# Kernel optimization log

Measured on AMD Instinct MI355X. Metric: run time of the kernel, lower is better.

Reference implementation:

```python
import jax, jax.numpy as jnp
import numpy as np

B, S, H = 2, 1024, 2048
NH, NKV, HD = 16, 4, 128           # heads, kv heads, head_dim
E, TOPK, NG, TOPKG, M = 8, 2, 4, 2, 512  # experts, top_k, n_group, topk_group, moe ffn dim
EPS = 1e-6
THETA = 10000.0
SCALE = HD ** -0.5
RSF = 1.0  # routed_scaling_factor


def rmsnorm(x, w):
    xf = x.astype(jnp.float32)
    var = jnp.mean(xf * xf, axis=-1, keepdims=True)
    return (w * (xf * jax.lax.rsqrt(var + EPS))).astype(x.dtype)


def rotate_half(x):
    x1, x2 = jnp.split(x, 2, axis=-1)
    return jnp.concatenate([-x2, x1], axis=-1)


def setup_inputs() -> dict:
    key = jax.random.key(0)
    ks = jax.random.split(key, 16)
    s = 0.02
    hidden_states = jax.random.normal(ks[0], (B, S, H), jnp.float32)
    pos = jnp.arange(S, dtype=jnp.float32)
    inv_freq = 1.0 / (THETA ** (jnp.arange(0, HD, 2, dtype=jnp.float32) / HD))
    freqs = jnp.outer(pos, inv_freq)                       # [S, HD/2]
    emb = jnp.concatenate([freqs, freqs], axis=-1)         # [S, HD]
    cos = jnp.broadcast_to(jnp.cos(emb)[None], (B, S, HD))
    sin = jnp.broadcast_to(jnp.sin(emb)[None], (B, S, HD))
    return {
        "hidden_states": hidden_states,
        "cos": cos,
        "sin": sin,
        "ln1_w": jnp.ones((H,), jnp.float32),
        "w_qkv": jax.random.normal(ks[1], ((NH + 2 * NKV) * HD, H), jnp.float32) * s,
        "q_ln_w": jnp.ones((HD,), jnp.float32),
        "k_ln_w": jnp.ones((HD,), jnp.float32),
        "w_dense": jax.random.normal(ks[2], (H, NH * HD), jnp.float32) * s,
        "ln2_w": jnp.ones((H,), jnp.float32),
        "gate_w": jax.random.normal(ks[3], (E, H), jnp.float32) * s,
        "gate_bias": jnp.zeros((E,), jnp.float32),
        "we_gate": jax.random.normal(ks[4], (E, M, H), jnp.float32) * s,
        "we_up": jax.random.normal(ks[5], (E, M, H), jnp.float32) * s,
        "we_down": jax.random.normal(ks[6], (E, H, M), jnp.float32) * s,
        "ws_gate": jax.random.normal(ks[7], (M, H), jnp.float32) * s,
        "ws_up": jax.random.normal(ks[8], (M, H), jnp.float32) * s,
        "ws_down": jax.random.normal(ks[9], (H, M), jnp.float32) * s,
    }


def reference(hidden_states, cos, sin, ln1_w, w_qkv, q_ln_w, k_ln_w, w_dense,
              ln2_w, gate_w, gate_bias, we_gate, we_up, we_down,
              ws_gate, ws_up, ws_down):
    # ---- attention block ----
    residual = hidden_states
    x = rmsnorm(hidden_states, ln1_w)
    qkv = jnp.einsum('bsh,oh->bso', x, w_qkv).reshape(B, S, NH + 2 * NKV, HD)
    q, k, v = jnp.split(qkv, [NH, NH + NKV], axis=2)
    q = q.transpose(0, 2, 1, 3)   # [B, NH,  S, HD]
    k = k.transpose(0, 2, 1, 3)   # [B, NKV, S, HD]
    v = v.transpose(0, 2, 1, 3)
    q = rmsnorm(q, q_ln_w)
    k = rmsnorm(k, k_ln_w)
    c, sn = cos[:, None], sin[:, None]  # [B,1,S,HD]
    q = q * c + rotate_half(q) * sn
    k = k * c + rotate_half(k) * sn
    n_rep = NH // NKV
    k = jnp.repeat(k, n_rep, axis=1)
    v = jnp.repeat(v, n_rep, axis=1)
    scores = jnp.einsum('bhqd,bhkd->bhqk', q, k) * SCALE
    attn = jax.nn.softmax(scores.astype(jnp.float32), axis=-1).astype(q.dtype)
    out = jnp.einsum('bhqk,bhkd->bhqd', attn, v)
    out = out.transpose(0, 2, 1, 3).reshape(B, S, NH * HD)
    attn_out = jnp.einsum('bso,ho->bsh', out, w_dense)
    hidden = residual + attn_out

    # ---- MoE block ----
    residual = hidden
    x = rmsnorm(hidden, ln2_w).reshape(B * S, H)
    T = B * S
    logits = jnp.einsum('th,eh->te', x.astype(jnp.float32), gate_w.astype(jnp.float32))
    scores = jax.nn.sigmoid(logits)
    scores_b = scores + gate_bias
    # group-limited routing: pick topk_group groups by sum of top-2 scores per group
    gsz = E // NG
    grp = scores_b.reshape(T, NG, gsz)
    top2 = jax.lax.top_k(grp, min(2, gsz))[0].sum(-1)      # [T, NG]
    _, gidx = jax.lax.top_k(top2, TOPKG)                   # [T, TOPKG]
    gmask = jnp.zeros((T, NG), scores.dtype).at[jnp.arange(T)[:, None], gidx].set(1.0)
    emask = jnp.repeat(gmask, gsz, axis=-1)                # [T, E]
    masked = jnp.where(emask > 0, scores_b, -jnp.inf)
    _, tidx = jax.lax.top_k(masked, TOPK)                  # [T, TOPK]
    tw = jnp.take_along_axis(scores, tidx, axis=-1)
    tw = tw / (tw.sum(-1, keepdims=True) + 1e-20) * RSF
    route = jnp.zeros((T, E), x.dtype).at[jnp.arange(T)[:, None], tidx].set(tw.astype(x.dtype))
    # dense all-expert compute, combined by (sparse) routing weights
    g = jnp.einsum('th,emh->tem', x, we_gate)
    u = jnp.einsum('th,emh->tem', x, we_up)
    he = jax.nn.silu(g) * u
    oe = jnp.einsum('tem,ehm->teh', he, we_down)
    moe = jnp.einsum('te,teh->th', route, oe)
    # shared expert
    sh = jnp.einsum('th,oh->to', jax.nn.silu(x @ ws_gate.T) * (x @ ws_up.T), ws_down)
    out = residual + (moe + sh).reshape(B, S, H)
    return out
```

## Files before the change

kernel.cpp:

```cpp
#include <hip/hip_runtime.h>
#include <cstdint>
#include <cstddef>

#define T_TOK 2048
#define H_DIM 2048
#define S_LEN 1024
#define HD 128
#define NH 16
#define NKV 4
#define QKV_O 3072
#define MM 512
#define EPS 1e-6f
#define ATT_SCALE 0.08838834764831845f

typedef __bf16 bf16x8 __attribute__((ext_vector_type(8)));
typedef __bf16 bf16x4 __attribute__((ext_vector_type(4)));
typedef float  f32x4  __attribute__((ext_vector_type(4)));

__device__ __forceinline__ __bf16 f2bf(float f) {
  unsigned u = __builtin_bit_cast(unsigned, f);
  u += 0x7fffu + ((u >> 16) & 1u);
  unsigned short h = (unsigned short)(u >> 16);
  return __builtin_bit_cast(__bf16, h);
}
__device__ __forceinline__ f32x4 fzero4() {
  f32x4 z; z[0] = 0.f; z[1] = 0.f; z[2] = 0.f; z[3] = 0.f; return z;
}
__device__ __forceinline__ void gld16(const __bf16* g, __bf16* l) {
  __builtin_amdgcn_global_load_lds(
      (const __attribute__((address_space(1))) unsigned int*)g,
      (__attribute__((address_space(3))) unsigned int*)l, 16, 0, 0);
}

__global__ __launch_bounds__(256) void wconv_k(
    const float* __restrict__ s0, const float* __restrict__ s1,
    const float* __restrict__ s2, const float* __restrict__ s3,
    const float* __restrict__ s4, const float* __restrict__ s5,
    const float* __restrict__ s6, const float* __restrict__ s7,
    __bf16* __restrict__ dst) {
  size_t e = ((size_t)blockIdx.x * 256 + threadIdx.x) * 4;
  const size_t E0 = 6291456, E1 = 10485760, E2 = 18874368, E3 = 27262976,
               E4 = 35651584, E5 = 36700160, E6 = 37748736;
  const float* src; size_t base;
  if      (e < E0) { src = s0; base = 0;  }
  else if (e < E1) { src = s1; base = E0; }
  else if (e < E2) { src = s2; base = E1; }
  else if (e < E3) { src = s3; base = E2; }
  else if (e < E4) { src = s4; base = E3; }
  else if (e < E5) { src = s5; base = E4; }
  else if (e < E6) { src = s6; base = E5; }
  else             { src = s7; base = E6; }
  float4 f = *(const float4*)(src + (e - base));
  bf16x4 o;
  o[0] = f2bf(f.x); o[1] = f2bf(f.y); o[2] = f2bf(f.z); o[3] = f2bf(f.w);
  *(bf16x4*)(dst + e) = o;
}

__global__ __launch_bounds__(256) void rmsnorm_k(const float* __restrict__ X,
                                                 const float* __restrict__ W,
                                                 __bf16* __restrict__ Y) {
  int t = blockIdx.x;
  int tid = threadIdx.x, lane = tid & 63, wid = tid >> 6;
  const float4* row = (const float4*)(X + (size_t)t * H_DIM);
  float4 v0 = row[tid], v1 = row[tid + 256];
  float ss = v0.x*v0.x + v0.y*v0.y + v0.z*v0.z + v0.w*v0.w
           + v1.x*v1.x + v1.y*v1.y + v1.z*v1.z + v1.w*v1.w;
  #pragma unroll
  for (int m = 1; m <= 32; m <<= 1) ss += __shfl_xor(ss, m, 64);
  __shared__ float red[4];
  if (lane == 0) red[wid] = ss;
  __syncthreads();
  float tot = red[0] + red[1] + red[2] + red[3];
  float sc = rsqrtf(tot * (1.f / H_DIM) + EPS);
  const float4* wp = (const float4*)W;
  float4 w0 = wp[tid], w1 = wp[tid + 256];
  bf16x4 o;
  o[0] = f2bf(v0.x*w0.x*sc); o[1] = f2bf(v0.y*w0.y*sc);
  o[2] = f2bf(v0.z*w0.z*sc); o[3] = f2bf(v0.w*w0.w*sc);
  *(bf16x4*)&Y[(size_t)t*H_DIM + tid*4] = o;
  o[0] = f2bf(v1.x*w1.x*sc); o[1] = f2bf(v1.y*w1.y*sc);
  o[2] = f2bf(v1.z*w1.z*sc); o[3] = f2bf(v1.w*w1.w*sc);
  *(bf16x4*)&Y[(size_t)t*H_DIM + 1024 + tid*4] = o;
}

template<int MODE>
__global__ __launch_bounds__(256) void gemm_nt(
    const __bf16* __restrict__ A, const __bf16* __restrict__ B,
    const __bf16* __restrict__ B2, float* __restrict__ C,
    const float* __restrict__ resid, const int* __restrict__ list,
    const float* __restrict__ wsl, const int* __restrict__ cnt,
    int N, int K) {
  int e  = (MODE == 2) ? (int)blockIdx.z : 0;
  int ne = (MODE == 2) ? ((e == 8) ? T_TOK : cnt[e]) : T_TOK;
  int m0 = blockIdx.y * 128;
  if (MODE == 2 && m0 >= ne) return;
  int n0 = blockIdx.x * 128;
  const __bf16* Ab = A;
  const __bf16* Bb = B;
  if (MODE == 2) {
    Ab = A + (size_t)e * T_TOK * MM;
    Bb = (e < 8) ? B + (size_t)e * H_DIM * MM : B2;
  }
  __shared__ __bf16 sA[128 * 64];
  __shared__ __bf16 sB[128 * 64];
  int tid = threadIdx.x, lane = tid & 63, wid = tid >> 6;
  int quad = lane >> 4, l16 = lane & 15;
  int wm = wid & 1, wn = wid >> 1;

  const __bf16* gA[4]; const __bf16* gB[4];
  #pragma unroll
  for (int i = 0; i < 4; i++) {
    int p = tid + 256 * i;
    int row = p >> 3, sc = p & 7, gc = sc ^ (row & 7);
    gA[i] = Ab + (size_t)(m0 + row) * K + gc * 8;
    gB[i] = Bb + (size_t)(n0 + row) * K + gc * 8;
  }
  f32x4 acc[4][4];
  #pragma unroll
  for (int i = 0; i < 4; i++)
    #pragma unroll
    for (int j = 0; j < 4; j++) acc[i][j] = fzero4();

  for (int k0 = 0; k0 < K; k0 += 64) {
    __syncthreads();
    #pragma unroll
    for (int i = 0; i < 4; i++) {
      gld16(gA[i] + k0, &sA[(tid + 256 * i) * 8]);
      gld16(gB[i] + k0, &sB[(tid + 256 * i) * 8]);
    }
    __syncthreads();
    #pragma unroll
    for (int ks = 0; ks < 64; ks += 32) {
      int cb = ks >> 3;
      bf16x8 aF[4], bF[4];
      #pragma unroll
      for (int mt = 0; mt < 4; mt++) {
        int row = wm * 64 + mt * 16 + l16;
        int pos = row * 8 + ((cb + quad) ^ (row & 7));
        aF[mt] = *(const bf16x8*)&sA[pos * 8];
      }
      #pragma unroll
      for (int nt = 0; nt < 4; nt++) {
        int row = wn * 64 + nt * 16 + l16;
        int pos = row * 8 + ((cb + quad) ^ (row & 7));
        bF[nt] = *(const bf16x8*)&sB[pos * 8];
      }
      #pragma unroll
      for (int mt = 0; mt < 4; mt++)
        #pragma unroll
        for (int nt = 0; nt < 4; nt++)
          acc[mt][nt] = __builtin_amdgcn_mfma_f32_16x16x32_bf16(
              aF[mt], bF[nt], acc[mt][nt], 0, 0, 0);
    }
  }
  #pragma unroll
  for (int mt = 0; mt < 4; mt++) {
    #pragma unroll
    for (int nt = 0; nt < 4; nt++) {
      #pragma unroll
      for (int r = 0; r < 4; r++) {
        int row_l = wm*64 + mt*16 + quad*4 + r;
        int col_l = wn*64 + nt*16 + l16;
        int grow = m0 + row_l, gcol = n0 + col_l;
        float val = acc[mt][nt][r];
        if (MODE == 0) {
          C[(size_t)grow * N + gcol] = val;
        } else if (MODE == 1) {
          C[(size_t)grow * H_DIM + gcol] = val + resid[(size_t)grow * H_DIM + gcol];
        } else {
          if (grow < ne) {
            int tk  = list[e * T_TOK + grow];
            float w = wsl[e * T_TOK + grow];
            atomicAdd(&C[(size_t)tk * H_DIM + gcol], val * w);
          }
        }
      }
    }
  }
}

__global__ __launch_bounds__(256) void rope_k(
    const float* __restrict__ qkv, const float* __restrict__ qlw,
    const float* __restrict__ klw, const float* __restrict__ cosp,
    const float* __restrict__ sinp, __bf16* __restrict__ qb,
    __bf16* __restrict__ kb, __bf16* __restrict__ vb) {
  int bid = blockIdx.x;
  int t = bid / 6;
  int head = (bid % 6) * 4 + (threadIdx.x >> 6);
  int b = t >> 10, s = t & 1023;
  int d = threadIdx.x & 63;
  const float* src = qkv + (size_t)t * QKV_O + head * HD;
  float x1 = src[d], x2 = src[d + 64];
  if (head < 20) {
    float ssq = x1*x1 + x2*x2;
    #pragma unroll
    for (int m = 1; m <= 32; m <<= 1) ssq += __shfl_xor(ssq, m, 64);
    float sc = rsqrtf(ssq * (1.f / HD) + EPS);
    const float* w = (head < 16) ? qlw : klw;
    x1 = x1 * sc * w[d];
    x2 = x2 * sc * w[d + 64];
    size_t cb = (size_t)t * HD;
    float c1 = cosp[cb + d], s1 = sinp[cb + d];
    float c2 = cosp[cb + d + 64], s2 = sinp[cb + d + 64];
    float o1 = x1 * c1 - x2 * s1;
    float o2 = x2 * c2 + x1 * s2;
    if (head < 16) {
      __bf16* dst = qb + (((size_t)(b * NH + head)) * S_LEN + s) * HD;
      dst[d] = f2bf(o1); dst[d + 64] = f2bf(o2);
    } else {
      int kv = head - 16;
      __bf16* dst = kb + (((size_t)(b * NKV + kv)) * S_LEN + s) * HD;
      dst[d] = f2bf(o1); dst[d + 64] = f2bf(o2);
    }
  } else {
    int kv = head - 20;
    __bf16* dst = vb + (((size_t)(b * NKV + kv)) * S_LEN + s) * HD;
    dst[d] = f2bf(x1); dst[d + 64] = f2bf(x2);
  }
}

__global__ __launch_bounds__(256) void vtrans_k(const __bf16* __restrict__ vb,
                                                __bf16* __restrict__ vt) {
  int s0 = blockIdx.x * 64, d0 = blockIdx.y * 64, g = blockIdx.z;
  __shared__ __bf16 sT[64 * 80];
  int tid = threadIdx.x;
  const __bf16* src = vb + (size_t)g * S_LEN * HD;
  #pragma unroll
  for (int i = 0; i < 2; i++) {
    int p = tid + 256 * i;
    int rs = p >> 3, cc = p & 7;
    bf16x8 v = *(const bf16x8*)(src + (size_t)(s0 + rs) * HD + d0 + cc * 8);
    #pragma unroll
    for (int j = 0; j < 8; j++) sT[(cc * 8 + j) * 80 + rs] = v[j];
  }
  __syncthreads();
  __bf16* dst = vt + (size_t)g * HD * S_LEN;
  #pragma unroll
  for (int i = 0; i < 2; i++) {
    int p = tid + 256 * i;
    int rd = p >> 3, cs = p & 7;
    bf16x8 v = *(const bf16x8*)&sT[rd * 80 + cs * 8];
    *(bf16x8*)(dst + (size_t)(d0 + rd) * S_LEN + s0 + cs * 8) = v;
  }
}

__global__ __launch_bounds__(256) void flash_k(
    const __bf16* __restrict__ qb, const __bf16* __restrict__ kb,
    const __bf16* __restrict__ vt, __bf16* __restrict__ outb) {
  int qt = blockIdx.x, bh = blockIdx.y;
  int b = bh >> 4, h = bh & 15, kv = h >> 2;
  int tid = threadIdx.x, lane = tid & 63, wid = tid >> 6;
  int quad = lane >> 4, l16 = lane & 15;
  __shared__ __bf16 sQ[64 * 128];
  __shared__ __bf16 sKP[64 * 128];
  __shared__ __bf16 sVt[128 * 64];
  __bf16* sK = sKP;
  __bf16* sP = sKP;

  const __bf16* qsrc = qb + (((size_t)(b * NH + h)) * S_LEN + qt * 64) * HD;
  #pragma unroll
  for (int i = 0; i < 4; i++) {
    int p = tid + 256 * i;
    int row = p >> 4, sc = p & 15, gc = sc ^ (row & 7);
    gld16(qsrc + (size_t)row * HD + gc * 8, &sQ[p * 8]);
  }
  const __bf16* kbase  = kb + ((size_t)(b * NKV + kv)) * S_LEN * HD;
  const __bf16* vtbase = vt + ((size_t)(b * NKV + kv)) * HD * S_LEN;
  const __bf16* gK[4]; const __bf16* gV[4];
  #pragma unroll
  for (int i = 0; i < 4; i++) {
    int p = tid + 256 * i;
    int rowk = p >> 4, sck = p & 15, gck = sck ^ (rowk & 7);
    gK[i] = kbase + (size_t)rowk * HD + gck * 8;
    int rowv = p >> 3, scv = p & 7, gcv = scv ^ (rowv & 7);
    gV[i] = vtbase + (size_t)rowv * S_LEN + gcv * 8;
  }
  float mrow[4], lrow[4];
  #pragma unroll
  for (int r = 0; r < 4; r++) { mrow[r] = -__builtin_inff(); lrow[r] = 0.f; }
  f32x4 accO[8];
  #pragma unroll
  for (int i = 0; i < 8; i++) accO[i] = fzero4();

  for (int kt = 0; kt < 16; kt++) {
    __syncthreads();
    #pragma unroll
    for (int i = 0; i < 4; i++) {
      gld16(gK[i] + (size_t)kt * 64 * HD, &sK[(tid + 256 * i) * 8]);
      gld16(gV[i] + kt * 64, &sVt[(tid + 256 * i) * 8]);
    }
    __syncthreads();
    f32x4 accS[4];
    #pragma unroll
    for (int jt = 0; jt < 4; jt++) accS[jt] = fzero4();
    int rowA = wid * 16 + l16;
    #pragma unroll
    for (int ks2 = 0; ks2 < 4; ks2++) {
      int posA = rowA * 16 + ((ks2 * 4 + quad) ^ (rowA & 7));
      bf16x8 aF = *(const bf16x8*)&sQ[posA * 8];
      #pragma unroll
      for (int jt = 0; jt < 4; jt++) {
        int rowB = jt * 16 + l16;
        int posB = rowB * 16 + ((ks2 * 4 + quad) ^ (rowB & 7));
        bf16x8 bF = *(const bf16x8*)&sK[posB * 8];
        accS[jt] = __builtin_amdgcn_mfma_f32_16x16x32_bf16(aF, bF, accS[jt], 0, 0, 0);
      }
    }
    float alpha[4];
    #pragma unroll
    for (int r = 0; r < 4; r++) {
      float mx = -__builtin_inff();
      #pragma unroll
      for (int jt = 0; jt < 4; jt++) {
        accS[jt][r] *= ATT_SCALE;
        mx = fmaxf(mx, accS[jt][r]);
      }
      #pragma unroll
      for (int m = 1; m <= 8; m <<= 1) mx = fmaxf(mx, __shfl_xor(mx, m, 64));
      float mn = fmaxf(mrow[r], mx);
      float al = __expf(mrow[r] - mn);
      float rs = 0.f;
      #pragma unroll
      for (int jt = 0; jt < 4; jt++) {
        float p = __expf(accS[jt][r] - mn);
        accS[jt][r] = p;
        rs += p;
      }
      #pragma unroll
      for (int m = 1; m <= 8; m <<= 1) rs += __shfl_xor(rs, m, 64);
      lrow[r] = lrow[r] * al + rs;
      mrow[r] = mn;
      alpha[r] = al;
    }
    #pragma unroll
    for (int nt = 0; nt < 8; nt++)
      #pragma unroll
      for (int r = 0; r < 4; r++) accO[nt][r] *= alpha[r];
    __syncthreads();
    #pragma unroll
    for (int jt = 0; jt < 4; jt++)
      #pragma unroll
      for (int r = 0; r < 4; r++)
        sP[(wid * 16 + quad * 4 + r) * 72 + jt * 16 + l16] = f2bf(accS[jt][r]);
    __syncthreads();
    #pragma unroll
    for (int ks2 = 0; ks2 < 2; ks2++) {
      bf16x8 aF = *(const bf16x8*)&sP[(wid * 16 + l16) * 72 + ks2 * 32 + quad * 8];
      #pragma unroll
      for (int nt = 0; nt < 8; nt++) {
        int rowB = nt * 16 + l16;
        int posB = rowB * 8 + ((ks2 * 4 + quad) ^ (rowB & 7));
        bf16x8 bF = *(const bf16x8*)&sVt[posB * 8];
        accO[nt] = __builtin_amdgcn_mfma_f32_16x16x32_bf16(aF, bF, accO[nt], 0, 0, 0);
      }
    }
  }
  #pragma unroll
  for (int nt = 0; nt < 8; nt++) {
    #pragma unroll
    for (int r = 0; r < 4; r++) {
      int srow = qt * 64 + wid * 16 + quad * 4 + r;
      float val = accO[nt][r] / lrow[r];
      outb[((size_t)(b * S_LEN + srow)) * H_DIM + h * HD + nt * 16 + l16] = f2bf(val);
    }
  }
}

__global__ __launch_bounds__(64) void router_k(
    const float* __restrict__ hid, const float* __restrict__ ln2w,
    const float* __restrict__ gw, const float* __restrict__ gb,
    int* __restrict__ cnt, int* __restrict__ list, float* __restrict__ wsl) {
  int t = blockIdx.x;
  int lane = threadIdx.x;
  const float* xr = hid + (size_t)t * H_DIM;
  float x[32];
  float ss = 0.f;
  #pragma unroll
  for (int j = 0; j < 32; j++) { x[j] = xr[j * 64 + lane]; ss += x[j] * x[j]; }
  #pragma unroll
  for (int m = 1; m <= 32; m <<= 1) ss += __shfl_xor(ss, m, 64);
  float sc = rsqrtf(ss * (1.f / H_DIM) + EPS);
  float xn[32];
  #pragma unroll
  for (int j = 0; j < 32; j++) xn[j] = x[j] * sc * ln2w[j * 64 + lane];
  float lg[8];
  #pragma unroll
  for (int e = 0; e < 8; e++) {
    float d = 0.f;
    #pragma unroll
    for (int j = 0; j < 32; j++) d += xn[j] * gw[(size_t)e * H_DIM + j * 64 + lane];
    #pragma unroll
    for (int m = 1; m <= 32; m <<= 1) d += __shfl_xor(d, m, 64);
    lg[e] = d;
  }
  float s[8], sb[8];
  #pragma unroll
  for (int e = 0; e < 8; e++) {
    s[e] = 1.f / (1.f + __expf(-lg[e]));
    sb[e] = s[e] + gb[e];
  }
  float gs[4];
  #pragma unroll
  for (int g = 0; g < 4; g++) gs[g] = sb[2 * g] + sb[2 * g + 1];
  int g1 = 0;
  for (int g = 1; g < 4; g++) if (gs[g] > gs[g1]) g1 = g;
  int g2 = -1;
  for (int g = 0; g < 4; g++) if (g != g1 && (g2 < 0 || gs[g] > gs[g2])) g2 = g;
  unsigned emask = (3u << (2 * g1)) | (3u << (2 * g2));
  int e1 = -1;
  for (int e = 0; e < 8; e++) if (((emask >> e) & 1u) && (e1 < 0 || sb[e] > sb[e1])) e1 = e;
  int e2 = -1;
  for (int e = 0; e < 8; e++) if (((emask >> e) & 1u) && e != e1 && (e2 < 0 || sb[e] > sb[e2])) e2 = e;
  float w1 = s[e1], w2 = s[e2];
  float dn = w1 + w2 + 1e-20f;
  w1 /= dn; w2 /= dn;
  if (lane == 0) {
    int p1 = atomicAdd(&cnt[e1], 1);
    list[e1 * T_TOK + p1] = t; wsl[e1 * T_TOK + p1] = w1;
    int p2 = atomicAdd(&cnt[e2], 1);
    list[e2 * T_TOK + p2] = t; wsl[e2 * T_TOK + p2] = w2;
    list[8 * T_TOK + t] = t; wsl[8 * T_TOK + t] = 1.f;
  }
}

__global__ __launch_bounds__(256) void gemm_gateup(
    const __bf16* __restrict__ X, const __bf16* __restrict__ weg,
    const __bf16* __restrict__ weu, const __bf16* __restrict__ wsg,
    const __bf16* __restrict__ wsu, const int* __restrict__ list,
    const int* __restrict__ cnt, __bf16* __restrict__ he) {
  int e = blockIdx.z;
  int ne = (e == 8) ? T_TOK : cnt[e];
  int m0 = blockIdx.y * 128;
  if (m0 >= ne) return;
  int n0 = blockIdx.x * 64;
  const __bf16* bg = (e < 8) ? weg + (size_t)e * MM * H_DIM : wsg;
  const __bf16* bu = (e < 8) ? weu + (size_t)e * MM * H_DIM : wsu;
  const int* lst = list + e * T_TOK;
  __shared__ __bf16 sA[128 * 64];
  __shared__ __bf16 sBg[64 * 64];
  __shared__ __bf16 sBu[64 * 64];
  int tid = threadIdx.x, lane = tid & 63, wid = tid >> 6;
  int quad = lane >> 4, l16 = lane & 15;

  const __bf16* gA[4]; const __bf16* gBg[2]; const __bf16* gBu[2];
  #pragma unroll
  for (int i = 0; i < 4; i++) {
    int p = tid + 256 * i;
    int row = p >> 3, sc = p & 7, gc = sc ^ (row & 7);
    int r = m0 + row; if (r >= ne) r = ne - 1;
    int tk = lst[r];
    gA[i] = X + (size_t)tk * H_DIM + gc * 8;
  }
  #pragma unroll
  for (int i = 0; i < 2; i++) {
    int p = tid + 256 * i;
    int row = p >> 3, sc = p & 7, gc = sc ^ (row & 7);
    gBg[i] = bg + (size_t)(n0 + row) * H_DIM + gc * 8;
    gBu[i] = bu + (size_t)(n0 + row) * H_DIM + gc * 8;
  }
  f32x4 ag[2][4], au[2][4];
  #pragma unroll
  for (int i = 0; i < 2; i++)
    #pragma unroll
    for (int j = 0; j < 4; j++) { ag[i][j] = fzero4(); au[i][j] = fzero4(); }

  for (int k0 = 0; k0 < H_DIM; k0 += 64) {
    __syncthreads();
    #pragma unroll
    for (int i = 0; i < 4; i++)
      gld16(gA[i] + k0, &sA[(tid + 256 * i) * 8]);
    #pragma unroll
    for (int i = 0; i < 2; i++) {
      gld16(gBg[i] + k0, &sBg[(tid + 256 * i) * 8]);
      gld16(gBu[i] + k0, &sBu[(tid + 256 * i) * 8]);
    }
    __syncthreads();
    #pragma unroll
    for (int ks = 0; ks < 64; ks += 32) {
      int cb = ks >> 3;
      bf16x8 aF[2], gF[4], uF[4];
      #pragma unroll
      for (int mt = 0; mt < 2; mt++) {
        int row = wid * 32 + mt * 16 + l16;
        int pos = row * 8 + ((cb + quad) ^ (row & 7));
        aF[mt] = *(const bf16x8*)&sA[pos * 8];
      }
      #pragma unroll
      for (int nt = 0; nt < 4; nt++) {
        int row = nt * 16 + l16;
        int pos = row * 8 + ((cb + quad) ^ (row & 7));
        gF[nt] = *(const bf16x8*)&sBg[pos * 8];
        uF[nt] = *(const bf16x8*)&sBu[pos * 8];
      }
      #pragma unroll
      for (int mt = 0; mt < 2; mt++)
        #pragma unroll
        for (int nt = 0; nt < 4; nt++) {
          ag[mt][nt] = __builtin_amdgcn_mfma_f32_16x16x32_bf16(aF[mt], gF[nt], ag[mt][nt], 0, 0, 0);
          au[mt][nt] = __builtin_amdgcn_mfma_f32_16x16x32_bf16(aF[mt], uF[nt], au[mt][nt], 0, 0, 0);
        }
    }
  }
  #pragma unroll
  for (int mt = 0; mt < 2; mt++) {
    #pragma unroll
    for (int nt = 0; nt < 4; nt++) {
      #pragma unroll
      for (int r = 0; r < 4; r++) {
        int row_l = wid * 32 + mt * 16 + quad * 4 + r;
        int grow = m0 + row_l;
        if (grow < ne) {
          float g = ag[mt][nt][r], u = au[mt][nt][r];
          float hv = g / (1.f + __expf(-g)) * u;
          he[((size_t)e * T_TOK + grow) * MM + n0 + nt * 16 + l16] = f2bf(hv);
        }
      }
    }
  }
}

extern "C" void kernel_launch(void* const* d_in, const int* in_sizes, int n_in,
                              void* d_out, int out_size, void* d_ws, size_t ws_size,
                              hipStream_t stream) {
  (void)in_sizes; (void)n_in; (void)out_size; (void)ws_size;
  const float* hs     = (const float*)d_in[0];
  const float* cosp   = (const float*)d_in[1];
  const float* sinp   = (const float*)d_in[2];
  const float* ln1w   = (const float*)d_in[3];
  const float* wqkv   = (const float*)d_in[4];
  const float* qlw    = (const float*)d_in[5];
  const float* klw    = (const float*)d_in[6];
  const float* wdense = (const float*)d_in[7];
  const float* ln2w   = (const float*)d_in[8];
  const float* gw     = (const float*)d_in[9];
  const float* gbias  = (const float*)d_in[10];
  const float* weg    = (const float*)d_in[11];
  const float* weu    = (const float*)d_in[12];
  const float* wed    = (const float*)d_in[13];
  const float* wsg    = (const float*)d_in[14];
  const float* wsu    = (const float*)d_in[15];
  const float* wsd    = (const float*)d_in[16];
  float* out = (float*)d_out;

  char* ws = (char*)d_ws;
  size_t off = 0;
  auto alloc = [&](size_t b) { char* p = ws + off; off += (b + 255) & ~(size_t)255; return p; };
  __bf16* wbf   = (__bf16*)alloc((size_t)38797312 * 2);
  __bf16* xb1   = (__bf16*)alloc((size_t)T_TOK * H_DIM * 2);
  float*  qkv32 = (float*) alloc((size_t)T_TOK * QKV_O * 4);
  __bf16* qb    = (__bf16*)alloc((size_t)2 * NH  * S_LEN * HD * 2);
  __bf16* kb    = (__bf16*)alloc((size_t)2 * NKV * S_LEN * HD * 2);
  __bf16* vb    = (__bf16*)alloc((size_t)2 * NKV * S_LEN * HD * 2);
  __bf16* vt    = (__bf16*)alloc((size_t)2 * NKV * S_LEN * HD * 2);
  __bf16* outb  = (__bf16*)alloc((size_t)T_TOK * H_DIM * 2);
  __bf16* xb2   = (__bf16*)alloc((size_t)T_TOK * H_DIM * 2);
  int*    cnt   = (int*)   alloc(256);
  int*    list  = (int*)   alloc((size_t)9 * T_TOK * 4);
  float*  wsl   = (float*) alloc((size_t)9 * T_TOK * 4);
  __bf16* he    = (__bf16*)qkv32;

  const __bf16* wqkv_bf   = wbf;
  const __bf16* wdense_bf = wbf + 6291456;
  const __bf16* weg_bf    = wbf + 10485760;
  const __bf16* weu_bf    = wbf + 18874368;
  const __bf16* wed_bf    = wbf + 27262976;
  const __bf16* wsg_bf    = wbf + 35651584;
  const __bf16* wsu_bf    = wbf + 36700160;
  const __bf16* wsd_bf    = wbf + 37748736;

  hipMemsetAsync(cnt, 0, 256, stream);
  wconv_k<<<37888, 256, 0, stream>>>(wqkv, wdense, weg, weu, wed, wsg, wsu, wsd, wbf);
  rmsnorm_k<<<T_TOK, 256, 0, stream>>>(hs, ln1w, xb1);
  gemm_nt<0><<<dim3(QKV_O / 128, T_TOK / 128), 256, 0, stream>>>(
      xb1, wqkv_bf, nullptr, qkv32, nullptr, nullptr, nullptr, nullptr, QKV_O, H_DIM);
  rope_k<<<T_TOK * 6, 256, 0, stream>>>(qkv32, qlw, klw, cosp, sinp, qb, kb, vb);
  vtrans_k<<<dim3(16, 2, 8), 256, 0, stream>>>(vb, vt);
  flash_k<<<dim3(S_LEN / 64, 2 * NH), 256, 0, stream>>>(qb, kb, vt, outb);
  gemm_nt<1><<<dim3(H_DIM / 128, T_TOK / 128), 256, 0, stream>>>(
      outb, wdense_bf, nullptr, out, hs, nullptr, nullptr, nullptr, H_DIM, H_DIM);
  rmsnorm_k<<<T_TOK, 256, 0, stream>>>(out, ln2w, xb2);
  router_k<<<T_TOK, 64, 0, stream>>>(out, ln2w, gw, gbias, cnt, list, wsl);
  gemm_gateup<<<dim3(MM / 64, T_TOK / 128, 9), 256, 0, stream>>>(
      xb2, weg_bf, weu_bf, wsg_bf, wsu_bf, list, cnt, he);
  gemm_nt<2><<<dim3(H_DIM / 128, T_TOK / 128, 9), 256, 0, stream>>>(
      he, wed_bf, wsd_bf, out, nullptr, list, wsl, cnt, H_DIM, MM);
}
```

Before: 548.2 us.

## Replace MoE down-proj atomics with bf16 slot buffer and combine kernel; bf16 QKV

The down-projection GEMM no longer does fp32 atomicAdd scatter into the output. Each token gets three bf16 slots (two routed experts plus the shared expert), indexed by a new per-assignment slot index written by the router, and a new combine kernel sums them into the residual output. The routing weight is now applied in the gate/up epilogue before bf16 rounding. The QKV GEMM also writes bf16 instead of fp32, which halves that intermediate's traffic, and the workspace is reused across stages. The cost is an extra kernel launch, extra buffer traffic, and more bf16 rounding of partial results.

```diff
diff --git a/kernel.cpp b/kernel.cpp
--- a/kernel.cpp
+++ b/kernel.cpp
@@ -87,9 +87,9 @@
 __global__ __launch_bounds__(256) void gemm_nt(
     const __bf16* __restrict__ A, const __bf16* __restrict__ B,
     const __bf16* __restrict__ B2, float* __restrict__ C,
-    const float* __restrict__ resid, const int* __restrict__ list,
-    const float* __restrict__ wsl, const int* __restrict__ cnt,
-    int N, int K) {
+    __bf16* __restrict__ OB, const float* __restrict__ resid,
+    const int* __restrict__ list, const signed char* __restrict__ jsl,
+    const int* __restrict__ cnt, int N, int K) {
   int e  = (MODE == 2) ? (int)blockIdx.z : 0;
   int ne = (MODE == 2) ? ((e == 8) ? T_TOK : cnt[e]) : T_TOK;
   int m0 = blockIdx.y * 128;
@@ -164,14 +164,14 @@
         int grow = m0 + row_l, gcol = n0 + col_l;
         float val = acc[mt][nt][r];
         if (MODE == 0) {
-          C[(size_t)grow * N + gcol] = val;
+          OB[(size_t)grow * N + gcol] = f2bf(val);
         } else if (MODE == 1) {
           C[(size_t)grow * H_DIM + gcol] = val + resid[(size_t)grow * H_DIM + gcol];
         } else {
           if (grow < ne) {
-            int tk  = list[e * T_TOK + grow];
-            float w = wsl[e * T_TOK + grow];
-            atomicAdd(&C[(size_t)tk * H_DIM + gcol], val * w);
+            int tk = list[e * T_TOK + grow];
+            int j  = (e == 8) ? 2 : (int)jsl[e * T_TOK + grow];
+            OB[((size_t)tk * 3 + j) * H_DIM + gcol] = f2bf(val);
           }
         }
       }
@@ -179,8 +179,28 @@
   }
 }
 
+__global__ __launch_bounds__(256) void combine_k(const __bf16* __restrict__ buf,
+                                                 float* __restrict__ out) {
+  int t = blockIdx.x, tid = threadIdx.x;
+  const __bf16* base = buf + (size_t)t * 3 * H_DIM;
+  bf16x8 v0 = *(const bf16x8*)(base + tid * 8);
+  bf16x8 v1 = *(const bf16x8*)(base + H_DIM + tid * 8);
+  bf16x8 v2 = *(const bf16x8*)(base + 2 * H_DIM + tid * 8);
+  float* o = out + (size_t)t * H_DIM + tid * 8;
+  float4 a = *(float4*)o, b = *(float4*)(o + 4);
+  a.x += (float)v0[0] + (float)v1[0] + (float)v2[0];
+  a.y += (float)v0[1] + (float)v1[1] + (float)v2[1];
+  a.z += (float)v0[2] + (float)v1[2] + (float)v2[2];
+  a.w += (float)v0[3] + (float)v1[3] + (float)v2[3];
+  b.x += (float)v0[4] + (float)v1[4] + (float)v2[4];
+  b.y += (float)v0[5] + (float)v1[5] + (float)v2[5];
+  b.z += (float)v0[6] + (float)v1[6] + (float)v2[6];
+  b.w += (float)v0[7] + (float)v1[7] + (float)v2[7];
+  *(float4*)o = a; *(float4*)(o + 4) = b;
+}
+
 __global__ __launch_bounds__(256) void rope_k(
-    const float* __restrict__ qkv, const float* __restrict__ qlw,
+    const __bf16* __restrict__ qkv, const float* __restrict__ qlw,
     const float* __restrict__ klw, const float* __restrict__ cosp,
     const float* __restrict__ sinp, __bf16* __restrict__ qb,
     __bf16* __restrict__ kb, __bf16* __restrict__ vb) {
@@ -189,8 +209,8 @@
   int head = (bid % 6) * 4 + (threadIdx.x >> 6);
   int b = t >> 10, s = t & 1023;
   int d = threadIdx.x & 63;
-  const float* src = qkv + (size_t)t * QKV_O + head * HD;
-  float x1 = src[d], x2 = src[d + 64];
+  const __bf16* src = qkv + (size_t)t * QKV_O + head * HD;
+  float x1 = (float)src[d], x2 = (float)src[d + 64];
   if (head < 20) {
     float ssq = x1*x1 + x2*x2;
     #pragma unroll
@@ -215,7 +235,7 @@
   } else {
     int kv = head - 20;
     __bf16* dst = vb + (((size_t)(b * NKV + kv)) * S_LEN + s) * HD;
-    dst[d] = f2bf(x1); dst[d + 64] = f2bf(x2);
+    dst[d] = src[d]; dst[d + 64] = src[d + 64];
   }
 }
 
@@ -369,7 +389,8 @@
 __global__ __launch_bounds__(64) void router_k(
     const float* __restrict__ hid, const float* __restrict__ ln2w,
     const float* __restrict__ gw, const float* __restrict__ gb,
-    int* __restrict__ cnt, int* __restrict__ list, float* __restrict__ wsl) {
+    int* __restrict__ cnt, int* __restrict__ list, float* __restrict__ wsl,
+    signed char* __restrict__ jsl) {
   int t = blockIdx.x;
   int lane = threadIdx.x;
   const float* xr = hid + (size_t)t * H_DIM;
@@ -416,9 +437,9 @@
   w1 /= dn; w2 /= dn;
   if (lane == 0) {
     int p1 = atomicAdd(&cnt[e1], 1);
-    list[e1 * T_TOK + p1] = t; wsl[e1 * T_TOK + p1] = w1;
+    list[e1 * T_TOK + p1] = t; wsl[e1 * T_TOK + p1] = w1; jsl[e1 * T_TOK + p1] = 0;
     int p2 = atomicAdd(&cnt[e2], 1);
-    list[e2 * T_TOK + p2] = t; wsl[e2 * T_TOK + p2] = w2;
+    list[e2 * T_TOK + p2] = t; wsl[e2 * T_TOK + p2] = w2; jsl[e2 * T_TOK + p2] = 1;
     list[8 * T_TOK + t] = t; wsl[8 * T_TOK + t] = 1.f;
   }
 }
@@ -427,7 +448,8 @@
     const __bf16* __restrict__ X, const __bf16* __restrict__ weg,
     const __bf16* __restrict__ weu, const __bf16* __restrict__ wsg,
     const __bf16* __restrict__ wsu, const int* __restrict__ list,
-    const int* __restrict__ cnt, __bf16* __restrict__ he) {
+    const float* __restrict__ wsl, const int* __restrict__ cnt,
+    __bf16* __restrict__ he) {
   int e = blockIdx.z;
   int ne = (e == 8) ? T_TOK : cnt[e];
   int m0 = blockIdx.y * 128;
@@ -512,6 +534,7 @@
         if (grow < ne) {
           float g = ag[mt][nt][r], u = au[mt][nt][r];
           float hv = g / (1.f + __expf(-g)) * u;
+          hv *= wsl[e * T_TOK + grow];
           he[((size_t)e * T_TOK + grow) * MM + n0 + nt * 16 + l16] = f2bf(hv);
         }
       }
@@ -547,7 +570,7 @@
   auto alloc = [&](size_t b) { char* p = ws + off; off += (b + 255) & ~(size_t)255; return p; };
   __bf16* wbf   = (__bf16*)alloc((size_t)38797312 * 2);
   __bf16* xb1   = (__bf16*)alloc((size_t)T_TOK * H_DIM * 2);
-  float*  qkv32 = (float*) alloc((size_t)T_TOK * QKV_O * 4);
+  __bf16* qreg  = (__bf16*)alloc((size_t)T_TOK * 3 * H_DIM * 2);
   __bf16* qb    = (__bf16*)alloc((size_t)2 * NH  * S_LEN * HD * 2);
   __bf16* kb    = (__bf16*)alloc((size_t)2 * NKV * S_LEN * HD * 2);
   __bf16* vb    = (__bf16*)alloc((size_t)2 * NKV * S_LEN * HD * 2);
@@ -557,7 +580,10 @@
   int*    cnt   = (int*)   alloc(256);
   int*    list  = (int*)   alloc((size_t)9 * T_TOK * 4);
   float*  wsl   = (float*) alloc((size_t)9 * T_TOK * 4);
-  __bf16* he    = (__bf16*)qkv32;
+  signed char* jsl = (signed char*)alloc((size_t)9 * T_TOK);
+  __bf16* qkvb  = qreg;
+  __bf16* buf   = qreg;
+  __bf16* he    = qb;
 
   const __bf16* wqkv_bf   = wbf;
   const __bf16* wdense_bf = wbf + 6291456;
@@ -572,16 +598,17 @@
   wconv_k<<<37888, 256, 0, stream>>>(wqkv, wdense, weg, weu, wed, wsg, wsu, wsd, wbf);
   rmsnorm_k<<<T_TOK, 256, 0, stream>>>(hs, ln1w, xb1);
   gemm_nt<0><<<dim3(QKV_O / 128, T_TOK / 128), 256, 0, stream>>>(
-      xb1, wqkv_bf, nullptr, qkv32, nullptr, nullptr, nullptr, nullptr, QKV_O, H_DIM);
-  rope_k<<<T_TOK * 6, 256, 0, stream>>>(qkv32, qlw, klw, cosp, sinp, qb, kb, vb);
+      xb1, wqkv_bf, nullptr, nullptr, qkvb, nullptr, nullptr, nullptr, nullptr, QKV_O, H_DIM);
+  rope_k<<<T_TOK * 6, 256, 0, stream>>>(qkvb, qlw, klw, cosp, sinp, qb, kb, vb);
   vtrans_k<<<dim3(16, 2, 8), 256, 0, stream>>>(vb, vt);
   flash_k<<<dim3(S_LEN / 64, 2 * NH), 256, 0, stream>>>(qb, kb, vt, outb);
   gemm_nt<1><<<dim3(H_DIM / 128, T_TOK / 128), 256, 0, stream>>>(
-      outb, wdense_bf, nullptr, out, hs, nullptr, nullptr, nullptr, H_DIM, H_DIM);
+      outb, wdense_bf, nullptr, out, nullptr, hs, nullptr, nullptr, nullptr, H_DIM, H_DIM);
   rmsnorm_k<<<T_TOK, 256, 0, stream>>>(out, ln2w, xb2);
-  router_k<<<T_TOK, 64, 0, stream>>>(out, ln2w, gw, gbias, cnt, list, wsl);
+  router_k<<<T_TOK, 64, 0, stream>>>(out, ln2w, gw, gbias, cnt, list, wsl, jsl);
   gemm_gateup<<<dim3(MM / 64, T_TOK / 128, 9), 256, 0, stream>>>(
-      xb2, weg_bf, weu_bf, wsg_bf, wsu_bf, list, cnt, he);
+      xb2, weg_bf, weu_bf, wsg_bf, wsu_bf, list, wsl, cnt, he);
   gemm_nt<2><<<dim3(H_DIM / 128, T_TOK / 128, 9), 256, 0, stream>>>(
-      he, wed_bf, wsd_bf, out, nullptr, list, wsl, cnt, H_DIM, MM);
-}
+      he, wed_bf, wsd_bf, nullptr, buf, nullptr, list, jsl, cnt, H_DIM, MM);
+  combine_k<<<T_TOK, 256, 0, stream>>>(buf, out);
+}
```

Result: faster. 528.3 us (-3.6%).
